# Kernel optimization log

Measured on AMD Instinct MI355X. Metric: run time of the kernel, lower is better.

Reference implementation:

```python
import jax, jax.numpy as jnp
import numpy as np

CHEBY_K = 3

def _normalize_adj(A):
    # A: [B, N, N]
    A = jnp.maximum(A, 0.0)
    N = A.shape[-1]
    A = A + jnp.eye(N, dtype=A.dtype)[None, :, :]
    D = jnp.maximum(A.sum(-1), 1e-6)          # [B, N]
    D_inv_sqrt = D ** -0.5
    return D_inv_sqrt[..., :, None] * A * D_inv_sqrt[..., None, :]


def setup_inputs() -> dict:
    key = jax.random.key(0)
    k1, k2, k3, k4, k5 = jax.random.split(key, 5)
    B, N, F_in, F_out, E = 16, 512, 64, 64, 16
    x = jax.random.normal(k1, (B, N, F_in), dtype=jnp.float32)
    emb = jax.random.normal(k2, (B, N, E), dtype=jnp.float32)
    A = jax.random.uniform(k3, (B, N, N), dtype=jnp.float32)
    # xavier-uniform-like init for pools
    lim_w = float(np.sqrt(6.0 / (E * CHEBY_K * F_in + F_out)))
    weights_pool = jax.random.uniform(k4, (E, CHEBY_K, F_in, F_out), dtype=jnp.float32,
                                      minval=-lim_w, maxval=lim_w)
    lim_b = float(np.sqrt(6.0 / (E + F_out)))
    bias_pool = jax.random.uniform(k5, (E, F_out), dtype=jnp.float32,
                                   minval=-lim_b, maxval=lim_b)
    return {"x": x, "emb": emb, "A": A,
            "weights_pool": weights_pool, "bias_pool": bias_pool}


def reference(x, emb, A, weights_pool, bias_pool):
    B, N, F_in = x.shape
    K = CHEBY_K
    A_hat = _normalize_adj(A)                                   # [B,N,N]
    t0 = jnp.broadcast_to(jnp.eye(N, dtype=x.dtype)[None], (B, N, N))
    supports = [t0, A_hat]
    for _ in range(2, K):
        supports.append(2.0 * jnp.matmul(A_hat, supports[-1]) - supports[-2])
    supports = jnp.stack(supports, axis=1)                      # [B,K,N,N]
    x_g = jnp.einsum('bknm,bmf->bknf', supports, x)             # [B,K,N,F_in]
    # fused per-node adaptive conv: avoids materializing [B,K,N,F_in,F_out]
    out = jnp.einsum('bknf,bne,ekfo->bno', x_g, emb, weights_pool)
    out = out + jnp.einsum('bne,eo->bno', emb, bias_pool)       # [B,N,F_out]
    return out
```

## Files before the change

kernel.cpp:

```cpp
#include <hip/hip_runtime.h>
#include <hip/hip_bf16.h>

#define NB 16
#define NN 512
#define NF 64
#define NE 16
#define NKF 192
#define NNODE (NB*NN)

typedef __hip_bfloat16 bf16;
typedef __attribute__((ext_vector_type(8))) short short8;
typedef __attribute__((ext_vector_type(4))) float f32x4;

typedef const __attribute__((address_space(1))) char gchar;
typedef __attribute__((address_space(3))) char lchar;

__device__ inline void gload16(const void* g, void* l) {
    __builtin_amdgcn_global_load_lds((gchar*)g, (lchar*)l, 16, 0, 0);
}

__device__ inline short f2bs(float f) {
    union { bf16 b; short s; } u; u.b = __float2bfloat16(f); return u.s;
}

__global__ __launch_bounds__(256) void k_pre(
    const float* __restrict__ A, const float* __restrict__ x,
    const float* __restrict__ Wp, float* __restrict__ dis,
    bf16* __restrict__ xg, bf16* __restrict__ xT, bf16* __restrict__ Bt) {
    __shared__ float Ts[64][66];
    int bid = blockIdx.x, tid = threadIdx.x;
    if (bid < 2048) {
        int row = bid * 4 + (tid >> 6);
        int lane = tid & 63;
        const float4* a = (const float4*)(A + (size_t)row * NN);
        float s = 0.f;
        #pragma unroll
        for (int j = 0; j < 2; ++j) {
            float4 v = a[lane + 64 * j];
            s += fmaxf(v.x, 0.f) + fmaxf(v.y, 0.f) + fmaxf(v.z, 0.f) + fmaxf(v.w, 0.f);
        }
        #pragma unroll
        for (int off = 32; off >= 1; off >>= 1) s += __shfl_down(s, off, 64);
        if (lane == 0) dis[row] = rsqrtf(fmaxf(s + 1.0f, 1e-6f));
    } else if (bid < 2176) {
        int node0 = (bid - 2048) * 64;
        int r = tid >> 2, f0 = (tid & 3) * 16;
        const float* xp = x + (size_t)(node0 + r) * NF + f0;
        float v[16];
        #pragma unroll
        for (int i = 0; i < 16; ++i) v[i] = xp[i];
        short8 p0, p1;
        #pragma unroll
        for (int i = 0; i < 8; ++i) { p0[i] = f2bs(v[i]); p1[i] = f2bs(v[8 + i]); }
        *(short8*)&xg[(size_t)(node0 + r) * NKF + f0] = p0;
        *(short8*)&xg[(size_t)(node0 + r) * NKF + f0 + 8] = p1;
        #pragma unroll
        for (int i = 0; i < 4; ++i)
            *(float4*)&Ts[r][f0 + i * 4] = *(const float4*)(v + i * 4);
        __syncthreads();
        int f = tid >> 2, nq0 = (tid & 3) * 16;
        int b = node0 >> 9, nloc = node0 & (NN - 1);
        bf16* xt = xT + (size_t)(b * NF + f) * NN + nloc + nq0;
        #pragma unroll
        for (int h = 0; h < 2; ++h) {
            short8 o;
            #pragma unroll
            for (int i = 0; i < 8; ++i) o[i] = f2bs(Ts[nq0 + h * 8 + i][f]);
            *(short8*)&xt[h * 8] = o;
        }
    } else {
        int q = bid - 2176;
        int e = q / 3, kt = q % 3;
        int r = tid >> 2, o0 = (tid & 3) * 16;
        const float* wp = Wp + (size_t)e * (NKF * NF) + (size_t)(kt * 64 + r) * NF + o0;
        #pragma unroll
        for (int i = 0; i < 4; ++i)
            *(float4*)&Ts[r][o0 + i * 4] = *(const float4*)(wp + i * 4);
        __syncthreads();
        int o = tid >> 2, r0 = (tid & 3) * 16;
        bf16* bt = Bt + (size_t)(e * 64 + o) * NKF + kt * 64 + r0;
        #pragma unroll
        for (int h = 0; h < 2; ++h) {
            short8 w;
            #pragma unroll
            for (int i = 0; i < 8; ++i) w[i] = f2bs(Ts[r0 + h * 8 + i][o]);
            *(short8*)&bt[h * 8] = w;
        }
    }
}

__global__ __launch_bounds__(256) void k_ahat(
    const float* __restrict__ A, const float* __restrict__ dis,
    bf16* __restrict__ Ah) {
    int tid = threadIdx.x;
    int row = blockIdx.x * 4 + (tid >> 6);
    int m0 = (tid & 63) * 8;
    int b = row >> 9, n = row & (NN - 1);
    const float* db = dis + b * NN;
    float dn = db[n];
    const float* ap = A + (size_t)row * NN + m0;
    float4 a0 = *(const float4*)ap, a1 = *(const float4*)(ap + 4);
    float4 d0 = *(const float4*)(db + m0), d1 = *(const float4*)(db + m0 + 4);
    float av[8] = {a0.x, a0.y, a0.z, a0.w, a1.x, a1.y, a1.z, a1.w};
    float dm[8] = {d0.x, d0.y, d0.z, d0.w, d1.x, d1.y, d1.z, d1.w};
    short8 o;
    #pragma unroll
    for (int i = 0; i < 8; ++i) {
        float v = fmaxf(av[i], 0.f) + ((n == m0 + i) ? 1.f : 0.f);
        o[i] = f2bs(v * dn * dm[i]);
    }
    *(short8*)&Ah[(size_t)row * NN + m0] = o;
}

template <int PASS>
__global__ __launch_bounds__(256) void k_spmm(
    const short* __restrict__ Ah, const short* __restrict__ Bsrc,
    const float* __restrict__ x, bf16* __restrict__ xg, bf16* __restrict__ y1T) {
    __shared__ short As[4 * 2048];
    __shared__ short Xs[4 * 2048];
    __shared__ float Cs[64][66];
    int tid = threadIdx.x, lane = tid & 63, w = tid >> 6;
    int n0 = blockIdx.x * 64, b = blockIdx.y;
    const short* Ab = Ah + (size_t)b * NN * NN;
    const short* Xb = Bsrc + (size_t)b * NF * NN;

    int sr = tid >> 2;
    int p  = tid & 3;
    int cA = p ^ ((sr >> 1) & 3);

    int fr = lane & 15, ak = lane >> 4;

    f32x4 acc[4] = {};

    for (int kt = 0; kt < 4; ++kt) {
        __syncthreads();
        #pragma unroll
        for (int kc = 0; kc < 4; ++kc) {
            int col = kt * 128 + kc * 32 + cA * 8;
            gload16(Ab + (size_t)(n0 + sr) * NN + col, As + kc * 2048 + tid * 8);
            gload16(Xb + (size_t)sr * NN + col,        Xs + kc * 2048 + tid * 8);
        }
        __syncthreads();
        int rA = 16 * w + fr;
        int swA = (ak ^ ((rA >> 1) & 3)) * 8;
        #pragma unroll
        for (int kc = 0; kc < 4; ++kc) {
            short8 afr = *(const short8*)&As[kc * 2048 + rA * 32 + swA];
            #pragma unroll
            for (int j = 0; j < 4; ++j) {
                int colr = 16 * j + fr;
                short8 bfr = *(const short8*)&Xs[kc * 2048 + colr * 32 +
                                                 ((ak ^ ((colr >> 1) & 3)) * 8)];
                acc[j] = __builtin_amdgcn_mfma_f32_16x16x32_bf16(afr, bfr, acc[j], 0, 0, 0);
            }
        }
    }

    #pragma unroll
    for (int j = 0; j < 4; ++j)
        #pragma unroll
        for (int r = 0; r < 4; ++r)
            Cs[16 * w + 4 * ak + r][16 * j + fr] = acc[j][r];
    __syncthreads();

    int nl = tid >> 2, f0 = (tid & 3) * 16;
    size_t node = (size_t)b * NN + n0 + nl;
    float cv[16];
    #pragma unroll
    for (int i = 0; i < 16; ++i) cv[i] = Cs[nl][f0 + i];
    if (PASS == 0) {
        short8 p0, p1;
        #pragma unroll
        for (int i = 0; i < 8; ++i) { p0[i] = f2bs(cv[i]); p1[i] = f2bs(cv[8 + i]); }
        *(short8*)&xg[node * NKF + 64 + f0] = p0;
        *(short8*)&xg[node * NKF + 64 + f0 + 8] = p1;
        int f = tid >> 2, nq0 = (tid & 3) * 16;
        bf16* yt = y1T + (size_t)(b * NF + f) * NN + n0 + nq0;
        #pragma unroll
        for (int h = 0; h < 2; ++h) {
            short8 o;
            #pragma unroll
            for (int i = 0; i < 8; ++i) o[i] = f2bs(Cs[nq0 + h * 8 + i][f]);
            *(short8*)&yt[h * 8] = o;
        }
    } else {
        const float* xp = x + node * NF + f0;
        short8 p0, p1;
        #pragma unroll
        for (int i = 0; i < 8; ++i) {
            p0[i] = f2bs(2.f * cv[i] - xp[i]);
            p1[i] = f2bs(2.f * cv[8 + i] - xp[8 + i]);
        }
        *(short8*)&xg[node * NKF + 128 + f0] = p0;
        *(short8*)&xg[node * NKF + 128 + f0 + 8] = p1;
    }
}

__global__ __launch_bounds__(256) void k_gemm(
    const short* __restrict__ xg, const short* __restrict__ Bt,
    bf16* __restrict__ t) {
    __shared__ short As[128 * 32];
    __shared__ short Bs[128 * 32];
    int tid = threadIdx.x;
    int lane = tid & 63;
    int w = tid >> 6;
    int n0 = blockIdx.x * 128;
    int c0 = blockIdx.y * 128;

    int rA0 = tid >> 2;
    int p   = tid & 3;
    int cA  = p ^ ((rA0 >> 1) & 3);

    int fr = lane & 15;
    int fc = ((lane >> 4) ^ ((fr >> 1) & 3)) * 8;

    f32x4 acc[4][4] = {};

    for (int kt = 0; kt < 6; ++kt) {
        __syncthreads();
        gload16(xg + (size_t)(n0 + rA0) * NKF + kt * 32 + cA * 8, As + tid * 8);
        gload16(xg + (size_t)(n0 + rA0 + 64) * NKF + kt * 32 + cA * 8, As + 2048 + tid * 8);
        gload16(Bt + (size_t)(c0 + rA0) * NKF + kt * 32 + cA * 8, Bs + tid * 8);
        gload16(Bt + (size_t)(c0 + rA0 + 64) * NKF + kt * 32 + cA * 8, Bs + 2048 + tid * 8);
        __syncthreads();

        int wr = w >> 1, wc = w & 1;
        short8 a[4], bfr[4];
        #pragma unroll
        for (int i = 0; i < 4; ++i)
            a[i] = *(const short8*)&As[(wr * 64 + i * 16 + fr) * 32 + fc];
        #pragma unroll
        for (int j = 0; j < 4; ++j)
            bfr[j] = *(const short8*)&Bs[(wc * 64 + j * 16 + fr) * 32 + fc];
        #pragma unroll
        for (int i = 0; i < 4; ++i)
            #pragma unroll
            for (int j = 0; j < 4; ++j)
                acc[i][j] = __builtin_amdgcn_mfma_f32_16x16x32_bf16(a[i], bfr[j], acc[i][j], 0, 0, 0);
    }

    int wr = w >> 1, wc = w & 1;
    #pragma unroll
    for (int i = 0; i < 4; ++i) {
        #pragma unroll
        for (int j = 0; j < 4; ++j) {
            #pragma unroll
            for (int r = 0; r < 4; ++r) {
                int m = n0 + wr * 64 + i * 16 + (lane >> 4) * 4 + r;
                int cc = c0 + wc * 64 + j * 16 + (lane & 15);
                t[(size_t)m * 1024 + cc] = __float2bfloat16(acc[i][j][r]);
            }
        }
    }
}

__global__ void k_reduce(const bf16* __restrict__ t, const float* __restrict__ emb,
                         const float* __restrict__ bp, float* __restrict__ out) {
    int gid = blockIdx.x * 256 + threadIdx.x;
    int node = gid >> 6, o = gid & 63;
    float s = 0.f;
    #pragma unroll
    for (int e = 0; e < NE; ++e) {
        float tv = __bfloat162float(t[(size_t)node * 1024 + e * 64 + o]);
        s = fmaf(emb[(size_t)node * NE + e], tv + bp[e * 64 + o], s);
    }
    out[gid] = s;
}

extern "C" void kernel_launch(void* const* d_in, const int* in_sizes, int n_in,
                              void* d_out, int out_size, void* d_ws, size_t ws_size,
                              hipStream_t stream) {
    const float* x   = (const float*)d_in[0];
    const float* emb = (const float*)d_in[1];
    const float* A   = (const float*)d_in[2];
    const float* Wp  = (const float*)d_in[3];
    const float* bp  = (const float*)d_in[4];
    float* out = (float*)d_out;

    float* ws  = (float*)d_ws;
    float* dis = ws;
    bf16*  xT  = (bf16*)(ws + 8192);
    bf16*  y1T = (bf16*)(ws + 270336);
    bf16*  xg  = (bf16*)(ws + 532480);
    bf16*  Bt  = (bf16*)(ws + 1318912);
    bf16*  Ah  = (bf16*)(ws + 1417216);
    bf16*  t   = (bf16*)(ws + 3514368);

    k_pre<<<2224, 256, 0, stream>>>(A, x, Wp, dis, xg, xT, Bt);
    k_ahat<<<2048, 256, 0, stream>>>(A, dis, Ah);
    dim3 g2(NN / 64, NB);
    k_spmm<0><<<g2, 256, 0, stream>>>((const short*)Ah, (const short*)xT, x, xg, y1T);
    k_spmm<1><<<g2, 256, 0, stream>>>((const short*)Ah, (const short*)y1T, x, xg, y1T);
    dim3 gg(NNODE / 128, 8);
    k_gemm<<<gg, 256, 0, stream>>>((const short*)xg, (const short*)Bt, t);
    k_reduce<<<NNODE * NF / 256, 256, 0, stream>>>(t, emb, bp, out);
}
```

Measured before the change: 42.08 us.

## Fuse second SpMM pass, feature GEMM and emb reduction into one kernel

Merges the second Chebyshev SpMM pass, the node-by-(E*F_out) GEMM and the emb-weighted reduction into a single kernel. Each 64-node block keeps its x_g tile in LDS and loops over the 16 embedding slices, streaming Bt slices and accumulating the emb-weighted output in registers. This removes the bf16 intermediate tensor t, its write and re-read, and two launches. In exchange the grid is only 128 blocks with a serial e-loop, larger LDS use and a barrier per iteration, so occupancy and parallelism drop.

```diff
diff --git a/kernel.cpp b/kernel.cpp
--- a/kernel.cpp
+++ b/kernel.cpp
@@ -112,10 +112,9 @@
     *(short8*)&Ah[(size_t)row * NN + m0] = o;
 }
 
-template <int PASS>
-__global__ __launch_bounds__(256) void k_spmm(
+__global__ __launch_bounds__(256) void k_spmm0(
     const short* __restrict__ Ah, const short* __restrict__ Bsrc,
-    const float* __restrict__ x, bf16* __restrict__ xg, bf16* __restrict__ y1T) {
+    bf16* __restrict__ xg, bf16* __restrict__ y1T) {
     __shared__ short As[4 * 2048];
     __shared__ short Xs[4 * 2048];
     __shared__ float Cs[64][66];
@@ -168,103 +167,139 @@
     float cv[16];
     #pragma unroll
     for (int i = 0; i < 16; ++i) cv[i] = Cs[nl][f0 + i];
-    if (PASS == 0) {
-        short8 p0, p1;
-        #pragma unroll
-        for (int i = 0; i < 8; ++i) { p0[i] = f2bs(cv[i]); p1[i] = f2bs(cv[8 + i]); }
-        *(short8*)&xg[node * NKF + 64 + f0] = p0;
-        *(short8*)&xg[node * NKF + 64 + f0 + 8] = p1;
-        int f = tid >> 2, nq0 = (tid & 3) * 16;
-        bf16* yt = y1T + (size_t)(b * NF + f) * NN + n0 + nq0;
-        #pragma unroll
-        for (int h = 0; h < 2; ++h) {
-            short8 o;
-            #pragma unroll
-            for (int i = 0; i < 8; ++i) o[i] = f2bs(Cs[nq0 + h * 8 + i][f]);
-            *(short8*)&yt[h * 8] = o;
-        }
-    } else {
-        const float* xp = x + node * NF + f0;
-        short8 p0, p1;
-        #pragma unroll
-        for (int i = 0; i < 8; ++i) {
-            p0[i] = f2bs(2.f * cv[i] - xp[i]);
-            p1[i] = f2bs(2.f * cv[8 + i] - xp[8 + i]);
-        }
-        *(short8*)&xg[node * NKF + 128 + f0] = p0;
-        *(short8*)&xg[node * NKF + 128 + f0 + 8] = p1;
-    }
-}
-
-__global__ __launch_bounds__(256) void k_gemm(
-    const short* __restrict__ xg, const short* __restrict__ Bt,
-    bf16* __restrict__ t) {
-    __shared__ short As[128 * 32];
-    __shared__ short Bs[128 * 32];
-    int tid = threadIdx.x;
-    int lane = tid & 63;
-    int w = tid >> 6;
-    int n0 = blockIdx.x * 128;
-    int c0 = blockIdx.y * 128;
-
-    int rA0 = tid >> 2;
-    int p   = tid & 3;
-    int cA  = p ^ ((rA0 >> 1) & 3);
-
-    int fr = lane & 15;
-    int fc = ((lane >> 4) ^ ((fr >> 1) & 3)) * 8;
-
-    f32x4 acc[4][4] = {};
-
-    for (int kt = 0; kt < 6; ++kt) {
-        __syncthreads();
-        gload16(xg + (size_t)(n0 + rA0) * NKF + kt * 32 + cA * 8, As + tid * 8);
-        gload16(xg + (size_t)(n0 + rA0 + 64) * NKF + kt * 32 + cA * 8, As + 2048 + tid * 8);
-        gload16(Bt + (size_t)(c0 + rA0) * NKF + kt * 32 + cA * 8, Bs + tid * 8);
-        gload16(Bt + (size_t)(c0 + rA0 + 64) * NKF + kt * 32 + cA * 8, Bs + 2048 + tid * 8);
-        __syncthreads();
-
-        int wr = w >> 1, wc = w & 1;
-        short8 a[4], bfr[4];
-        #pragma unroll
-        for (int i = 0; i < 4; ++i)
-            a[i] = *(const short8*)&As[(wr * 64 + i * 16 + fr) * 32 + fc];
-        #pragma unroll
-        for (int j = 0; j < 4; ++j)
-            bfr[j] = *(const short8*)&Bs[(wc * 64 + j * 16 + fr) * 32 + fc];
-        #pragma unroll
-        for (int i = 0; i < 4; ++i)
-            #pragma unroll
-            for (int j = 0; j < 4; ++j)
-                acc[i][j] = __builtin_amdgcn_mfma_f32_16x16x32_bf16(a[i], bfr[j], acc[i][j], 0, 0, 0);
-    }
-
-    int wr = w >> 1, wc = w & 1;
-    #pragma unroll
-    for (int i = 0; i < 4; ++i) {
+    short8 p0, p1;
+    #pragma unroll
+    for (int i = 0; i < 8; ++i) { p0[i] = f2bs(cv[i]); p1[i] = f2bs(cv[8 + i]); }
+    *(short8*)&xg[node * NKF + 64 + f0] = p0;
+    *(short8*)&xg[node * NKF + 64 + f0 + 8] = p1;
+    int f = tid >> 2, nq0 = (tid & 3) * 16;
+    bf16* yt = y1T + (size_t)(b * NF + f) * NN + n0 + nq0;
+    #pragma unroll
+    for (int h = 0; h < 2; ++h) {
+        short8 o;
+        #pragma unroll
+        for (int i = 0; i < 8; ++i) o[i] = f2bs(Cs[nq0 + h * 8 + i][f]);
+        *(short8*)&yt[h * 8] = o;
+    }
+}
+
+__global__ __launch_bounds__(256) void k_fuse(
+    const short* __restrict__ Ah, const short* __restrict__ y1T,
+    const float* __restrict__ x, const short* __restrict__ xg,
+    const short* __restrict__ Bt, const float* __restrict__ emb,
+    const float* __restrict__ bp, float* __restrict__ out) {
+    __shared__ short As[6 * 2048];
+    __shared__ short Bs[6 * 2048];
+    __shared__ float Es[64 * NE];
+    __shared__ float Ps[NE * 64];
+    int tid = threadIdx.x, lane = tid & 63, w = tid >> 6;
+    int n0 = blockIdx.x * 64, b = blockIdx.y;
+    const short* Ab = Ah + (size_t)b * NN * NN;
+    const short* Xb = y1T + (size_t)b * NF * NN;
+
+    int sr = tid >> 2;
+    int p  = tid & 3;
+    int cA = p ^ ((sr >> 1) & 3);
+
+    int fr = lane & 15, ak = lane >> 4;
+
+    f32x4 acc[4] = {};
+    for (int kt = 0; kt < 4; ++kt) {
+        __syncthreads();
+        #pragma unroll
+        for (int kc = 0; kc < 4; ++kc) {
+            int col = kt * 128 + kc * 32 + cA * 8;
+            gload16(Ab + (size_t)(n0 + sr) * NN + col, As + kc * 2048 + tid * 8);
+            gload16(Xb + (size_t)sr * NN + col,        Bs + kc * 2048 + tid * 8);
+        }
+        __syncthreads();
+        int rA = 16 * w + fr;
+        int swA = (ak ^ ((rA >> 1) & 3)) * 8;
+        #pragma unroll
+        for (int kc = 0; kc < 4; ++kc) {
+            short8 afr = *(const short8*)&As[kc * 2048 + rA * 32 + swA];
+            #pragma unroll
+            for (int j = 0; j < 4; ++j) {
+                int colr = 16 * j + fr;
+                short8 bfr = *(const short8*)&Bs[kc * 2048 + colr * 32 +
+                                                 ((ak ^ ((colr >> 1) & 3)) * 8)];
+                acc[j] = __builtin_amdgcn_mfma_f32_16x16x32_bf16(afr, bfr, acc[j], 0, 0, 0);
+            }
+        }
+    }
+    __syncthreads();
+
+    #pragma unroll
+    for (int kk = 0; kk < 4; ++kk)
+        gload16(xg + (size_t)(b * NN + n0 + sr) * NKF + kk * 32 + cA * 8,
+                As + kk * 2048 + tid * 8);
+    #pragma unroll
+    for (int j = 0; j < 4; ++j) {
+        #pragma unroll
+        for (int r = 0; r < 4; ++r) {
+            int row = 16 * w + 4 * ak + r;
+            int col = 16 * j + fr;
+            float xv = x[((size_t)b * NN + n0 + row) * NF + col];
+            short v = f2bs(2.f * acc[j][r] - xv);
+            int kk   = 4 + (col >> 5);
+            int c    = (col & 31) >> 3;
+            int slot = c ^ ((row >> 1) & 3);
+            As[kk * 2048 + row * 32 + slot * 8 + (fr & 7)] = v;
+        }
+    }
+    {
+        const float* eb = emb + (size_t)(b * NN + n0) * NE;
+        #pragma unroll
+        for (int i = 0; i < 4; ++i) Es[tid + i * 256] = eb[tid + i * 256];
+        #pragma unroll
+        for (int i = 0; i < 4; ++i) Ps[tid + i * 256] = bp[tid + i * 256];
+    }
+    __syncthreads();
+
+    int arow = 16 * w + fr;
+    int swA2 = (ak ^ ((arow >> 1) & 3)) * 8;
+    short8 afr[6];
+    #pragma unroll
+    for (int kk = 0; kk < 6; ++kk)
+        afr[kk] = *(const short8*)&As[kk * 2048 + arow * 32 + swA2];
+
+    float oacc[4][4] = {};
+    for (int e = 0; e < NE; ++e) {
+        #pragma unroll
+        for (int kk = 0; kk < 6; ++kk)
+            gload16(Bt + (size_t)(e * 64 + sr) * NKF + kk * 32 + cA * 8,
+                    Bs + kk * 2048 + tid * 8);
+        __syncthreads();
+        f32x4 pe[4] = {};
+        #pragma unroll
+        for (int kk = 0; kk < 6; ++kk) {
+            #pragma unroll
+            for (int j = 0; j < 4; ++j) {
+                int brow = 16 * j + fr;
+                short8 bfr = *(const short8*)&Bs[kk * 2048 + brow * 32 +
+                                                 ((ak ^ ((brow >> 1) & 3)) * 8)];
+                pe[j] = __builtin_amdgcn_mfma_f32_16x16x32_bf16(afr[kk], bfr, pe[j], 0, 0, 0);
+            }
+        }
         #pragma unroll
         for (int j = 0; j < 4; ++j) {
+            float bv = Ps[e * 64 + 16 * j + fr];
             #pragma unroll
             for (int r = 0; r < 4; ++r) {
-                int m = n0 + wr * 64 + i * 16 + (lane >> 4) * 4 + r;
-                int cc = c0 + wc * 64 + j * 16 + (lane & 15);
-                t[(size_t)m * 1024 + cc] = __float2bfloat16(acc[i][j][r]);
+                int nl = 16 * w + 4 * ak + r;
+                oacc[j][r] = fmaf(Es[nl * NE + e], pe[j][r] + bv, oacc[j][r]);
             }
         }
-    }
-}
-
-__global__ void k_reduce(const bf16* __restrict__ t, const float* __restrict__ emb,
-                         const float* __restrict__ bp, float* __restrict__ out) {
-    int gid = blockIdx.x * 256 + threadIdx.x;
-    int node = gid >> 6, o = gid & 63;
-    float s = 0.f;
-    #pragma unroll
-    for (int e = 0; e < NE; ++e) {
-        float tv = __bfloat162float(t[(size_t)node * 1024 + e * 64 + o]);
-        s = fmaf(emb[(size_t)node * NE + e], tv + bp[e * 64 + o], s);
-    }
-    out[gid] = s;
+        __syncthreads();
+    }
+
+    #pragma unroll
+    for (int j = 0; j < 4; ++j)
+        #pragma unroll
+        for (int r = 0; r < 4; ++r) {
+            int node = b * NN + n0 + 16 * w + 4 * ak + r;
+            out[(size_t)node * NF + 16 * j + fr] = oacc[j][r];
+        }
 }
 
 extern "C" void kernel_launch(void* const* d_in, const int* in_sizes, int n_in,
@@ -284,14 +319,11 @@
     bf16*  xg  = (bf16*)(ws + 532480);
     bf16*  Bt  = (bf16*)(ws + 1318912);
     bf16*  Ah  = (bf16*)(ws + 1417216);
-    bf16*  t   = (bf16*)(ws + 3514368);
 
     k_pre<<<2224, 256, 0, stream>>>(A, x, Wp, dis, xg, xT, Bt);
     k_ahat<<<2048, 256, 0, stream>>>(A, dis, Ah);
     dim3 g2(NN / 64, NB);
-    k_spmm<0><<<g2, 256, 0, stream>>>((const short*)Ah, (const short*)xT, x, xg, y1T);
-    k_spmm<1><<<g2, 256, 0, stream>>>((const short*)Ah, (const short*)y1T, x, xg, y1T);
-    dim3 gg(NNODE / 128, 8);
-    k_gemm<<<gg, 256, 0, stream>>>((const short*)xg, (const short*)Bt, t);
-    k_reduce<<<NNODE * NF / 256, 256, 0, stream>>>(t, emb, bp, out);
-}
+    k_spmm0<<<g2, 256, 0, stream>>>((const short*)Ah, (const short*)xT, xg, y1T);
+    k_fuse<<<g2, 256, 0, stream>>>((const short*)Ah, (const short*)y1T, x,
+                                   (const short*)xg, (const short*)Bt, emb, bp, out);
+}
```

Measured after the change: 44.60 us. +6.0%, slower.
